# Performance work log

Hardware: AMD Instinct MI355X
Metric: run time of the kernel (lower is better)

The kernel has to match this reference:

```python
import jax, jax.numpy as jnp
import numpy as np

N_NODES = 100000
N_EDGES = 3200000
IN_F, HID, OUT = 24, 64, 1


def _gcn_conv(x, W, b, src, dst, norm, n):
    # x: [N, Fin] -> h: [N, Fout]; PyG GCNConv: lin first, then normalized aggregation, then bias
    h = x @ W                                    # [N, Fout]
    msg = h[src] * norm[:, None]                 # [E+N, Fout] gathered, norm-weighted messages
    agg = jax.ops.segment_sum(msg, dst, num_segments=n)  # scatter-add to targets
    return agg + b


def setup_inputs() -> dict:
    key = jax.random.key(0)
    k1, k2, k3, k4 = jax.random.split(key, 4)
    x = jax.random.normal(k1, (N_NODES, IN_F), dtype=jnp.float32)
    edge_index = jax.random.randint(k2, (2, N_EDGES), 0, N_NODES, dtype=jnp.int64)
    # Glorot-ish init for weights
    W1 = jax.random.normal(k3, (IN_F, HID), dtype=jnp.float32) / np.sqrt(IN_F)
    b1 = jnp.zeros((HID,), dtype=jnp.float32)
    W2 = jax.random.normal(k4, (HID, OUT), dtype=jnp.float32) / np.sqrt(HID)
    b2 = jnp.zeros((OUT,), dtype=jnp.float32)
    return {"x": x, "edge_index": edge_index, "W1": W1, "b1": b1, "W2": W2, "b2": b2}


def reference(x, edge_index, W1, b1, W2, b2):
    n = x.shape[0]
    # add self-loops (PyG GCNConv default)
    loops = jnp.arange(n, dtype=edge_index.dtype)
    src = jnp.concatenate([edge_index[0], loops])
    dst = jnp.concatenate([edge_index[1], loops])
    # symmetric normalization: deg over targets of A+I, norm_e = d^-1/2[src] * d^-1/2[dst]
    deg = jax.ops.segment_sum(jnp.ones_like(dst, dtype=x.dtype), dst, num_segments=n)
    dinv = jnp.where(deg > 0, jax.lax.rsqrt(deg), 0.0)
    norm = dinv[src] * dinv[dst]
    h = _gcn_conv(x, W1, b1, src, dst, norm, n)
    h = jax.nn.relu(h)
    # F.dropout with training=self.training -> identity in eval mode (reference runs eval)
    out = _gcn_conv(h, W2, b2, src, dst, norm, n)
    return out
```

## Files before the change

kernel.cpp:

```cpp
#include <hip/hip_runtime.h>
#include <hip/hip_fp16.h>

#define IN_F 24
#define HID 64
#define NB 512
#define NPB 256
#define GSZ_MAX 256
#define PBUF 7168
#define SRC_BITS 17

typedef unsigned int u32;

__device__ __forceinline__ int bucket_lo(int b, int n) {
    return (int)(((long long)b * n + NB - 1) / NB);
}

__global__ __launch_bounds__(256) void k_pcount(const int* __restrict__ dst,
                                                u32* __restrict__ pc, int e, int n) {
    __shared__ u32 h[NB];
    for (int j = threadIdx.x; j < NB; j += 256) h[j] = 0;
    __syncthreads();
    int blk = blockIdx.x;
    long long begin = (long long)e * blk / NPB;
    long long end   = (long long)e * (blk + 1) / NPB;
    for (long long i = begin + threadIdx.x; i < end; i += 256) {
        int k = (int)((long long)dst[i] * NB / n);
        atomicAdd(&h[k], 1u);
    }
    __syncthreads();
    for (int j = threadIdx.x; j < NB; j += 256) pc[(size_t)blk * NB + j] = h[j];
}

__global__ __launch_bounds__(256) void k_pscan_a(u32* __restrict__ pc,
                                                 u32* __restrict__ colsum) {
    __shared__ u32 ps[256];
    int t = blockIdx.x;
    int tid = threadIdx.x;
    u32 v = pc[(size_t)tid * NB + t];
    ps[tid] = v;
    __syncthreads();
    for (int off = 1; off < 256; off <<= 1) {
        u32 v2 = (tid >= off) ? ps[tid - off] : 0;
        __syncthreads();
        ps[tid] += v2;
        __syncthreads();
    }
    pc[(size_t)tid * NB + t] = ps[tid] - v;
    if (tid == 255) colsum[t] = ps[255];
}

__global__ void k_pscan_b(const u32* __restrict__ colsum, u32* __restrict__ basep) {
    __shared__ u32 s[NB];
    int t = threadIdx.x;
    u32 v = colsum[t];
    s[t] = v;
    __syncthreads();
    for (int off = 1; off < NB; off <<= 1) {
        u32 v2 = (t >= off) ? s[t - off] : 0;
        __syncthreads();
        s[t] += v2;
        __syncthreads();
    }
    basep[t] = s[t] - v;
}

__global__ __launch_bounds__(256) void k_part(const int* __restrict__ src,
                                              const int* __restrict__ dst,
                                              const u32* __restrict__ pc,
                                              const u32* __restrict__ basep,
                                              u32* __restrict__ pairs, int e, int n) {
    __shared__ u32 cur[NB];
    int blk = (blockIdx.x & 7) * (NPB / 8) + (blockIdx.x >> 3);
    for (int j = threadIdx.x; j < NB; j += 256)
        cur[j] = pc[(size_t)blk * NB + j] + basep[j];
    __syncthreads();
    long long begin = (long long)e * blk / NPB;
    long long end   = (long long)e * (blk + 1) / NPB;
    for (long long i = begin + threadIdx.x; i < end; i += 256) {
        int d = dst[i];
        int sv = src[i];
        int k = (int)((long long)d * NB / n);
        u32 loc = (u32)(d - bucket_lo(k, n));
        u32 pos = atomicAdd(&cur[k], 1u);
        pairs[pos] = (loc << SRC_BITS) | (u32)sv;
    }
}

__global__ __launch_bounds__(256) void k_bucket(const u32* __restrict__ pairs,
                                                const u32* __restrict__ basep,
                                                const float* __restrict__ x,
                                                int* __restrict__ cnt,
                                                int* __restrict__ row_start,
                                                float* __restrict__ dinv,
                                                int* __restrict__ csr_src,
                                                __half2* __restrict__ xs2, int e, int n) {
    __shared__ u32 pbuf[PBUF];
    __shared__ u32 h[GSZ_MAX];
    __shared__ u32 cur[GSZ_MAX];
    __shared__ u32 sc[GSZ_MAX];
    __shared__ float dloc[GSZ_MAX];
    int b = blockIdx.x;
    if (b == 0 && threadIdx.x < 12)
        xs2[(long long)n * 12 + threadIdx.x] = __floats2half2_rn(0.0f, 0.0f);
    int lo = bucket_lo(b, n);
    int hi = bucket_lo(b + 1, n);
    int gsz = hi - lo;
    u32 start = basep[b];
    u32 endp = (b + 1 < NB) ? basep[b + 1] : (u32)e;
    int nbp = (int)(endp - start);
    for (int j = threadIdx.x; j < GSZ_MAX; j += 256) h[j] = 0;
    __syncthreads();
    int stored = nbp < PBUF ? nbp : PBUF;
    for (int i = threadIdx.x; i < stored; i += 256) {
        u32 p = pairs[start + i];
        pbuf[i] = p;
        atomicAdd(&h[p >> SRC_BITS], 1u);
    }
    for (int i = PBUF + threadIdx.x; i < nbp; i += 256) {
        atomicAdd(&h[pairs[start + i] >> SRC_BITS], 1u);
    }
    __syncthreads();
    int t = threadIdx.x;
    u32 v = h[t];
    sc[t] = v;
    __syncthreads();
    for (int off = 1; off < 256; off <<= 1) {
        u32 v2 = (t >= off) ? sc[t - off] : 0;
        __syncthreads();
        sc[t] += v2;
        __syncthreads();
    }
    u32 excl = sc[t] - v;
    if (t < gsz) {
        float dv = rsqrtf((float)(v + 1));
        cnt[lo + t] = (int)v;
        row_start[lo + t] = (int)(start + excl);
        dinv[lo + t] = dv;
        dloc[t] = dv;
        cur[t] = excl;
    }
    __syncthreads();
    for (int i = threadIdx.x; i < stored; i += 256) {
        u32 p = pbuf[i];
        u32 pos = atomicAdd(&cur[p >> SRC_BITS], 1u);
        csr_src[start + pos] = (int)(p & ((1u << SRC_BITS) - 1));
    }
    for (int i = PBUF + threadIdx.x; i < nbp; i += 256) {
        u32 p = pairs[start + i];
        u32 pos = atomicAdd(&cur[p >> SRC_BITS], 1u);
        csr_src[start + pos] = (int)(p & ((1u << SRC_BITS) - 1));
    }
    const float2* xf = (const float2*)(x + (long long)lo * IN_F);
    for (int i = threadIdx.x; i < gsz * 12; i += 256) {
        float2 vv = xf[i];
        float dn = dloc[i / 12];
        xs2[(long long)lo * 12 + i] = __floats2half2_rn(vv.x * dn, vv.y * dn);
    }
}

__global__ __launch_bounds__(256) void k_agg_hz(const float* __restrict__ x,
                                                const __half2* __restrict__ xs2,
                                                const float* __restrict__ dinv,
                                                const int* __restrict__ row_start,
                                                const int* __restrict__ cnt,
                                                const int* __restrict__ csr_src,
                                                const float* __restrict__ W1,
                                                const float* __restrict__ b1,
                                                const float* __restrict__ W2,
                                                float* __restrict__ zs, int n) {
    __shared__ float w[IN_F * HID];
    __shared__ float w2s[HID];
    __shared__ float b1s[HID];
    for (int j = threadIdx.x; j < IN_F * HID; j += 256) w[j] = W1[j];
    if (threadIdx.x < HID) { w2s[threadIdx.x] = W2[threadIdx.x]; b1s[threadIdx.x] = b1[threadIdx.x]; }
    __syncthreads();
    int g = threadIdx.x >> 4;
    int f2 = threadIdx.x & 15;
    int node = blockIdx.x * 16 + g;
    if (node >= n) return;
    float dn = dinv[node];
    float ax = 0.0f, ay = 0.0f;
    if (f2 < 12) {
        int row = row_start[node];
        int c = cnt[node];
        const int* cp = csr_src + row;
        int nbatch = (c + 15) >> 4;
        float px0 = 0.0f, px1 = 0.0f, px2 = 0.0f, px3 = 0.0f;
        float py0 = 0.0f, py1 = 0.0f, py2 = 0.0f, py3 = 0.0f;
        int s[16];
        if (nbatch > 0) {
#pragma unroll
            for (int t = 0; t < 16; ++t) {
                int tmp = cp[t];
                s[t] = (t < c) ? tmp : n;
            }
        }
        for (int bb = 0; bb < nbatch; ++bb) {
            __half2 h[16];
#pragma unroll
            for (int t = 0; t < 16; ++t) h[t] = xs2[s[t] * 12 + f2];
            int s2[16];
            int base2 = (bb + 1) << 4;
            if (bb + 1 < nbatch) {
#pragma unroll
                for (int t = 0; t < 16; ++t) {
                    int tmp = cp[base2 + t];
                    s2[t] = (base2 + t < c) ? tmp : n;
                }
            }
#pragma unroll
            for (int t = 0; t < 16; t += 4) {
                float2 f0 = __half22float2(h[t]);
                float2 f1 = __half22float2(h[t + 1]);
                float2 f2v = __half22float2(h[t + 2]);
                float2 f3 = __half22float2(h[t + 3]);
                px0 += f0.x; px1 += f1.x; px2 += f2v.x; px3 += f3.x;
                py0 += f0.y; py1 += f1.y; py2 += f2v.y; py3 += f3.y;
            }
            if (bb + 1 < nbatch) {
#pragma unroll
                for (int t = 0; t < 16; ++t) s[t] = s2[t];
            }
        }
        ax = (px0 + px1) + (px2 + px3);
        ay = (py0 + py1) + (py2 + py3);
        float sx = x[(long long)node * IN_F + 2 * f2];
        float sy = x[(long long)node * IN_F + 2 * f2 + 1];
        ax = (ax + sx * dn) * dn;
        ay = (ay + sy * dn) * dn;
    }
    int fb = f2 * 4;
    float h0 = b1s[fb], h1 = b1s[fb + 1], h2 = b1s[fb + 2], h3 = b1s[fb + 3];
#pragma unroll
    for (int k = 0; k < IN_F; ++k) {
        float xv = __shfl((k & 1) ? ay : ax, k >> 1, 16);
        const float* wr = w + k * HID + fb;
        h0 += xv * wr[0];
        h1 += xv * wr[1];
        h2 += xv * wr[2];
        h3 += xv * wr[3];
    }
    float p = fmaxf(h0, 0.0f) * w2s[fb] + fmaxf(h1, 0.0f) * w2s[fb + 1]
            + fmaxf(h2, 0.0f) * w2s[fb + 2] + fmaxf(h3, 0.0f) * w2s[fb + 3];
    p += __shfl_down(p, 8, 16);
    p += __shfl_down(p, 4, 16);
    p += __shfl_down(p, 2, 16);
    p += __shfl_down(p, 1, 16);
    if (f2 == 0) zs[node] = p * dn;
}

__global__ void k_out(const float* __restrict__ zs, const float* __restrict__ dinv,
                      const int* __restrict__ row_start, const int* __restrict__ cnt,
                      const int* __restrict__ csr_src, const float* __restrict__ b2,
                      float* __restrict__ out, int n) {
    int t = blockIdx.x * blockDim.x + threadIdx.x;
    int node = t >> 4;
    int lane = t & 15;
    if (node >= n) return;
    int row = row_start[node];
    int c = cnt[node];
    float v = 0.0f;
    for (int j = lane; j < c; j += 16) {
        v += zs[csr_src[row + j]];
    }
    v += __shfl_down(v, 8, 16);
    v += __shfl_down(v, 4, 16);
    v += __shfl_down(v, 2, 16);
    v += __shfl_down(v, 1, 16);
    if (lane == 0) {
        out[node] = b2[0] + dinv[node] * (zs[node] + v);
    }
}

extern "C" void kernel_launch(void* const* d_in, const int* in_sizes, int n_in,
                              void* d_out, int out_size, void* d_ws, size_t ws_size,
                              hipStream_t stream) {
    const float* x   = (const float*)d_in[0];
    const int*   ei  = (const int*)d_in[1];
    const float* W1  = (const float*)d_in[2];
    const float* b1  = (const float*)d_in[3];
    const float* W2  = (const float*)d_in[4];
    const float* b2  = (const float*)d_in[5];
    float* out = (float*)d_out;

    const int n = in_sizes[0] / IN_F;
    const int e = in_sizes[1] / 2;
    const int* src = ei;
    const int* dst = ei + e;

    const int B = 256;

    char* base = (char*)d_ws;
    u32* pairs     = (u32*)base;
    float* zs      = (float*)base;
    size_t ov = ((size_t)e * 4 + 255) & ~(size_t)255;
    char* after    = base + ov;
    int* cnt       = (int*)after;
    int* row_start = cnt + n;
    int* csr_src   = row_start + n;
    float* dinv    = (float*)(csr_src + e);
    __half* xs     = (__half*)(dinv + n);
    u32* pc        = (u32*)(xs + (size_t)n * IN_F + 32);
    u32* colsum    = pc + (size_t)NPB * NB;
    u32* basep     = colsum + NB;

    k_pcount<<<NPB, B, 0, stream>>>(dst, pc, e, n);
    k_pscan_a<<<NB, B, 0, stream>>>(pc, colsum);
    k_pscan_b<<<1, NB, 0, stream>>>(colsum, basep);
    k_part<<<NPB, B, 0, stream>>>(src, dst, pc, basep, pairs, e, n);
    k_bucket<<<NB, B, 0, stream>>>(pairs, basep, x, cnt, row_start, dinv, csr_src,
                                   (__half2*)xs, e, n);

    k_agg_hz<<<(n + 15) / 16, B, 0, stream>>>(x, (const __half2*)xs, dinv,
                                              row_start, cnt, csr_src,
                                              W1, b1, W2, zs, n);

    const long long n16 = (long long)n * 16;
    k_out<<<(int)((n16 + B - 1) / B), B, 0, stream>>>(zs, dinv, row_start, cnt, csr_src, b2, out, n);
}
```

Baseline: 231.4 us.

## Use 8 lanes per node with 8-byte feature gathers in layer-1 aggregation

```diff
diff --git a/kernel.cpp b/kernel.cpp
--- a/kernel.cpp
+++ b/kernel.cpp
@@ -100,8 +100,6 @@
     __shared__ u32 sc[GSZ_MAX];
     __shared__ float dloc[GSZ_MAX];
     int b = blockIdx.x;
-    if (b == 0 && threadIdx.x < 12)
-        xs2[(long long)n * 12 + threadIdx.x] = __floats2half2_rn(0.0f, 0.0f);
     int lo = bucket_lo(b, n);
     int hi = bucket_lo(b + 1, n);
     int gsz = hi - lo;
@@ -174,79 +172,93 @@
     for (int j = threadIdx.x; j < IN_F * HID; j += 256) w[j] = W1[j];
     if (threadIdx.x < HID) { w2s[threadIdx.x] = W2[threadIdx.x]; b1s[threadIdx.x] = b1[threadIdx.x]; }
     __syncthreads();
-    int g = threadIdx.x >> 4;
-    int f2 = threadIdx.x & 15;
-    int node = blockIdx.x * 16 + g;
+    int g = threadIdx.x >> 3;
+    int f4 = threadIdx.x & 7;
+    int node = blockIdx.x * 32 + g;
     if (node >= n) return;
     float dn = dinv[node];
-    float ax = 0.0f, ay = 0.0f;
-    if (f2 < 12) {
+    const uint2* xq = (const uint2*)xs2;
+    float ax0 = 0.0f, ay0 = 0.0f, ax1 = 0.0f, ay1 = 0.0f;
+    if (f4 < 6) {
         int row = row_start[node];
         int c = cnt[node];
-        const int* cp = csr_src + row;
-        int nbatch = (c + 15) >> 4;
-        float px0 = 0.0f, px1 = 0.0f, px2 = 0.0f, px3 = 0.0f;
-        float py0 = 0.0f, py1 = 0.0f, py2 = 0.0f, py3 = 0.0f;
-        int s[16];
-        if (nbatch > 0) {
-#pragma unroll
-            for (int t = 0; t < 16; ++t) {
-                int tmp = cp[t];
-                s[t] = (t < c) ? tmp : n;
+        float a0 = 0.0f, b0 = 0.0f, c0 = 0.0f, d0 = 0.0f;
+        float a1 = 0.0f, b1v = 0.0f, c1 = 0.0f, d1 = 0.0f;
+        int j = 0;
+        for (; j + 16 <= c; j += 16) {
+            const int* cp = csr_src + row + j;
+            int s[16];
+#pragma unroll
+            for (int t = 0; t < 16; ++t) s[t] = cp[t];
+            uint2 u[16];
+#pragma unroll
+            for (int t = 0; t < 16; ++t) u[t] = xq[(size_t)((u32)s[t] * 6u + (u32)f4)];
+#pragma unroll
+            for (int t = 0; t < 16; t += 2) {
+                float2 e0 = __half22float2(__builtin_bit_cast(__half2, u[t].x));
+                float2 e1 = __half22float2(__builtin_bit_cast(__half2, u[t].y));
+                float2 o0 = __half22float2(__builtin_bit_cast(__half2, u[t + 1].x));
+                float2 o1 = __half22float2(__builtin_bit_cast(__half2, u[t + 1].y));
+                a0 += e0.x; b0 += e0.y; c0 += e1.x; d0 += e1.y;
+                a1 += o0.x; b1v += o0.y; c1 += o1.x; d1 += o1.y;
             }
         }
-        for (int bb = 0; bb < nbatch; ++bb) {
-            __half2 h[16];
-#pragma unroll
-            for (int t = 0; t < 16; ++t) h[t] = xs2[s[t] * 12 + f2];
-            int s2[16];
-            int base2 = (bb + 1) << 4;
-            if (bb + 1 < nbatch) {
-#pragma unroll
-                for (int t = 0; t < 16; ++t) {
-                    int tmp = cp[base2 + t];
-                    s2[t] = (base2 + t < c) ? tmp : n;
-                }
-            }
-#pragma unroll
-            for (int t = 0; t < 16; t += 4) {
-                float2 f0 = __half22float2(h[t]);
-                float2 f1 = __half22float2(h[t + 1]);
-                float2 f2v = __half22float2(h[t + 2]);
-                float2 f3 = __half22float2(h[t + 3]);
-                px0 += f0.x; px1 += f1.x; px2 += f2v.x; px3 += f3.x;
-                py0 += f0.y; py1 += f1.y; py2 += f2v.y; py3 += f3.y;
-            }
-            if (bb + 1 < nbatch) {
-#pragma unroll
-                for (int t = 0; t < 16; ++t) s[t] = s2[t];
+        for (; j + 8 <= c; j += 8) {
+            const int* cp = csr_src + row + j;
+            int s[8];
+#pragma unroll
+            for (int t = 0; t < 8; ++t) s[t] = cp[t];
+            uint2 u[8];
+#pragma unroll
+            for (int t = 0; t < 8; ++t) u[t] = xq[(size_t)((u32)s[t] * 6u + (u32)f4)];
+#pragma unroll
+            for (int t = 0; t < 8; t += 2) {
+                float2 e0 = __half22float2(__builtin_bit_cast(__half2, u[t].x));
+                float2 e1 = __half22float2(__builtin_bit_cast(__half2, u[t].y));
+                float2 o0 = __half22float2(__builtin_bit_cast(__half2, u[t + 1].x));
+                float2 o1 = __half22float2(__builtin_bit_cast(__half2, u[t + 1].y));
+                a0 += e0.x; b0 += e0.y; c0 += e1.x; d0 += e1.y;
+                a1 += o0.x; b1v += o0.y; c1 += o1.x; d1 += o1.y;
             }
         }
-        ax = (px0 + px1) + (px2 + px3);
-        ay = (py0 + py1) + (py2 + py3);
-        float sx = x[(long long)node * IN_F + 2 * f2];
-        float sy = x[(long long)node * IN_F + 2 * f2 + 1];
-        ax = (ax + sx * dn) * dn;
-        ay = (ay + sy * dn) * dn;
-    }
-    int fb = f2 * 4;
-    float h0 = b1s[fb], h1 = b1s[fb + 1], h2 = b1s[fb + 2], h3 = b1s[fb + 3];
+        for (; j < c; ++j) {
+            int s = csr_src[row + j];
+            uint2 u = xq[(size_t)((u32)s * 6u + (u32)f4)];
+            float2 e0 = __half22float2(__builtin_bit_cast(__half2, u.x));
+            float2 e1 = __half22float2(__builtin_bit_cast(__half2, u.y));
+            a0 += e0.x; b0 += e0.y; c0 += e1.x; d0 += e1.y;
+        }
+        ax0 = a0 + a1; ay0 = b0 + b1v; ax1 = c0 + c1; ay1 = d0 + d1;
+        float4 sx4 = *(const float4*)(x + (long long)node * IN_F + 4 * f4);
+        ax0 = (ax0 + sx4.x * dn) * dn;
+        ay0 = (ay0 + sx4.y * dn) * dn;
+        ax1 = (ax1 + sx4.z * dn) * dn;
+        ay1 = (ay1 + sx4.w * dn) * dn;
+    }
+    int fb = f4 * 8;
+    float h[8];
+#pragma unroll
+    for (int jj = 0; jj < 8; ++jj) h[jj] = b1s[fb + jj];
 #pragma unroll
     for (int k = 0; k < IN_F; ++k) {
-        float xv = __shfl((k & 1) ? ay : ax, k >> 1, 16);
+        int sl = k >> 2;
+        int r = k & 3;
+        float xv;
+        if (r == 0)      xv = __shfl(ax0, sl, 8);
+        else if (r == 1) xv = __shfl(ay0, sl, 8);
+        else if (r == 2) xv = __shfl(ax1, sl, 8);
+        else             xv = __shfl(ay1, sl, 8);
         const float* wr = w + k * HID + fb;
-        h0 += xv * wr[0];
-        h1 += xv * wr[1];
-        h2 += xv * wr[2];
-        h3 += xv * wr[3];
-    }
-    float p = fmaxf(h0, 0.0f) * w2s[fb] + fmaxf(h1, 0.0f) * w2s[fb + 1]
-            + fmaxf(h2, 0.0f) * w2s[fb + 2] + fmaxf(h3, 0.0f) * w2s[fb + 3];
-    p += __shfl_down(p, 8, 16);
-    p += __shfl_down(p, 4, 16);
-    p += __shfl_down(p, 2, 16);
-    p += __shfl_down(p, 1, 16);
-    if (f2 == 0) zs[node] = p * dn;
+#pragma unroll
+        for (int jj = 0; jj < 8; ++jj) h[jj] += xv * wr[jj];
+    }
+    float p = 0.0f;
+#pragma unroll
+    for (int jj = 0; jj < 8; ++jj) p += fmaxf(h[jj], 0.0f) * w2s[fb + jj];
+    p += __shfl_down(p, 4, 8);
+    p += __shfl_down(p, 2, 8);
+    p += __shfl_down(p, 1, 8);
+    if (f4 == 0) zs[node] = p * dn;
 }
 
 __global__ void k_out(const float* __restrict__ zs, const float* __restrict__ dinv,
@@ -300,7 +312,7 @@
     int* csr_src   = row_start + n;
     float* dinv    = (float*)(csr_src + e);
     __half* xs     = (__half*)(dinv + n);
-    u32* pc        = (u32*)(xs + (size_t)n * IN_F + 32);
+    u32* pc        = (u32*)(xs + (size_t)n * IN_F);
     u32* colsum    = pc + (size_t)NPB * NB;
     u32* basep     = colsum + NB;
 
@@ -311,7 +323,7 @@
     k_bucket<<<NB, B, 0, stream>>>(pairs, basep, x, cnt, row_start, dinv, csr_src,
                                    (__half2*)xs, e, n);
 
-    k_agg_hz<<<(n + 15) / 16, B, 0, stream>>>(x, (const __half2*)xs, dinv,
+    k_agg_hz<<<(n + 31) / 32, B, 0, stream>>>(x, (const __half2*)xs, dinv,
                                               row_start, cnt, csr_src,
                                               W1, b1, W2, zs, n);
 
```

Measured after the change: 218.1 us. -5.8%, faster.
